# Kernel optimization log

Measured on AMD Instinct MI355X. Metric: run time of the kernel, lower is better.

## Reference

```python
import jax, jax.numpy as jnp
import numpy as np

DIM = 768
N_HEADS = 12
HEAD_DIM = DIM // N_HEADS

def setup_inputs() -> dict:
    key = jax.random.key(0)
    ks = jax.random.split(key, 5)
    B, N = 8, 1024
    s = 0.02
    x = jax.random.normal(ks[0], (B, N, DIM), dtype=jnp.float32)
    W_qkv = jax.random.normal(ks[1], (DIM, 3 * DIM), dtype=jnp.float32) * s
    b_qkv = jnp.zeros((3 * DIM,), dtype=jnp.float32)
    W_proj = jax.random.normal(ks[2], (DIM, DIM), dtype=jnp.float32) * s
    b_proj = jnp.zeros((DIM,), dtype=jnp.float32)
    return {"x": x, "W_qkv": W_qkv, "b_qkv": b_qkv, "W_proj": W_proj, "b_proj": b_proj}

def reference(x, W_qkv, b_qkv, W_proj, b_proj):
    B, N, D = x.shape
    qkv = x @ W_qkv + b_qkv                                   # [B,N,3D]
    qkv = qkv.reshape(B, N, 3, N_HEADS, HEAD_DIM)
    q, k, v = qkv[:, :, 0], qkv[:, :, 1], qkv[:, :, 2]        # [B,N,H,hd]
    q = q.transpose(0, 2, 1, 3)                               # [B,H,N,hd]
    k = k.transpose(0, 2, 1, 3)
    v = v.transpose(0, 2, 1, 3)
    scores = jnp.einsum('bhqd,bhkd->bhqk', q, k) / jnp.sqrt(jnp.float32(HEAD_DIM))
    attn = jax.nn.softmax(scores, axis=-1)
    out = jnp.einsum('bhqk,bhkd->bhqd', attn, v)              # [B,H,N,hd]
    out = out.transpose(0, 2, 1, 3).reshape(B, N, D)
    return out @ W_proj + b_proj
```

## Files before the change

### kernel.cpp

```cpp
#include <hip/hip_runtime.h>
#include <hip/hip_bf16.h>


typedef __bf16 bf16x8 __attribute__((ext_vector_type(8)));
typedef float f32x4 __attribute__((ext_vector_type(4)));

#define MFMA16(a, b, c) __builtin_amdgcn_mfma_f32_16x16x32_bf16(a, b, c, 0, 0, 0)

__device__ inline __bf16 to_bf16(float f) {
  __hip_bfloat16 h = __float2bfloat16(f);
  return *reinterpret_cast<__bf16*>(&h);
}

__device__ __forceinline__ void gload16(const void* g, void* l) {
  __builtin_amdgcn_global_load_lds(
      (const __attribute__((address_space(1))) unsigned int*)(unsigned long long)g,
      (__attribute__((address_space(3))) unsigned int*)(unsigned long long)l,
      16, 0, 0);
}

__global__ void ws_diag_kernel(float* out, int n, float val) {
  int i = blockIdx.x * 256 + threadIdx.x;
  if (i < n) out[i] = val;
}

__global__ __launch_bounds__(256) void convert_x_kernel(
    const float* __restrict__ x, __hip_bfloat16* __restrict__ xc, int n8) {
  int i = blockIdx.x * 256 + threadIdx.x;
  if (i >= n8) return;
  float4 a = ((const float4*)x)[i * 2], b = ((const float4*)x)[i * 2 + 1];
  __hip_bfloat16 o[8] = {__float2bfloat16(a.x), __float2bfloat16(a.y),
                         __float2bfloat16(a.z), __float2bfloat16(a.w),
                         __float2bfloat16(b.x), __float2bfloat16(b.y),
                         __float2bfloat16(b.z), __float2bfloat16(b.w)};
  *(int4*)(xc + (size_t)i * 8) = *(const int4*)o;
}

__global__ void convert_transpose_kernel(const float* __restrict__ W,
                                         __hip_bfloat16* __restrict__ Wt,
                                         int rows, int cols) {
  __shared__ __hip_bfloat16 tile[32][33];
  const int tc = blockIdx.x * 32, tr = blockIdx.y * 32;
  const int tx = threadIdx.x, ty = threadIdx.y;
#pragma unroll
  for (int i = 0; i < 4; ++i) {
    int r = ty + i * 8;
    tile[r][tx] = __float2bfloat16(W[(size_t)(tr + r) * cols + tc + tx]);
  }
  __syncthreads();
#pragma unroll
  for (int i = 0; i < 4; ++i) {
    int r = ty + i * 8;
    Wt[(size_t)(tc + r) * rows + tr + tx] = tile[tx][r];
  }
}

__global__ __launch_bounds__(256) void vtrans_kernel(
    const __hip_bfloat16* __restrict__ Vrow, __hip_bfloat16* __restrict__ Vt) {
  constexpr int LP = 72;
  __shared__ __bf16 tile[64 * LP];
  const int tid = threadIdx.x;
  const int bh = blockIdx.x;
  const int n0 = blockIdx.y * 64;
  const size_t base = (size_t)bh << 16;
#pragma unroll
  for (int i = 0; i < 2; ++i) {
    int s = tid + 256 * i;
    int r = s >> 3, c8 = (s & 7) * 8;
    *(int4*)(&tile[r * LP + c8]) =
        *(const int4*)(Vrow + base + (size_t)(n0 + r) * 64 + c8);
  }
  __syncthreads();
#pragma unroll
  for (int i = 0; i < 2; ++i) {
    int s = tid + 256 * i;
    int d = s >> 3, n8 = (s & 7) * 8;
    __bf16 o[8];
#pragma unroll
    for (int j = 0; j < 8; ++j) o[j] = tile[(n8 + j) * LP + d];
    *(int4*)(Vt + base + ((size_t)d << 10) + n0 + n8) = *(const int4*)o;
  }
}

constexpr int GK = 768;

__global__ __launch_bounds__(256) void gemm_qkv_kernel(
    const __hip_bfloat16* __restrict__ A,
    const __hip_bfloat16* __restrict__ Bt,
    const float* __restrict__ bias,
    __hip_bfloat16* __restrict__ Qw,
    __hip_bfloat16* __restrict__ Kw,
    __hip_bfloat16* __restrict__ Vw) {
  __shared__ __align__(16) __bf16 As[128 * 32];
  __shared__ __align__(16) __bf16 Bs[128 * 32];
  const int tid = threadIdx.x;
  const int lane = tid & 63, wave = tid >> 6;
  const int wr = wave >> 1, wc = wave & 1;
  const int m0 = blockIdx.x * 128, n0 = blockIdx.y * 128;
  const int fr = lane & 15, q4 = lane >> 4;

  const int r4 = lane >> 2, c8 = (lane & 3) * 8;
  const __hip_bfloat16* ga0 = A + (size_t)(m0 + wave * 32 + r4) * GK + c8;
  const __hip_bfloat16* gb0 = Bt + (size_t)(n0 + wave * 32 + r4) * GK + c8;
  __bf16* la0 = &As[wave * 1024];
  __bf16* lb0 = &Bs[wave * 1024];

  f32x4 acc[4][4] = {};

  for (int kt = 0; kt < GK / 32; ++kt) {
    __syncthreads();
    gload16(ga0 + kt * 32, la0);
    gload16(ga0 + kt * 32 + 16 * GK, la0 + 512);
    gload16(gb0 + kt * 32, lb0);
    gload16(gb0 + kt * 32 + 16 * GK, lb0 + 512);
    __syncthreads();
    bf16x8 af[4], bfr[4];
#pragma unroll
    for (int i = 0; i < 4; ++i)
      af[i] = *(const bf16x8*)(&As[(wr * 64 + i * 16 + fr) * 32 + q4 * 8]);
#pragma unroll
    for (int j = 0; j < 4; ++j)
      bfr[j] = *(const bf16x8*)(&Bs[(wc * 64 + j * 16 + fr) * 32 + q4 * 8]);
#pragma unroll
    for (int i = 0; i < 4; ++i)
#pragma unroll
      for (int j = 0; j < 4; ++j)
        acc[i][j] = MFMA16(af[i], bfr[j], acc[i][j]);
  }

#pragma unroll
  for (int j = 0; j < 4; ++j) {
    int col = n0 + wc * 64 + j * 16 + fr;
    int which = col / 768;
    int rem = col - which * 768;
    int h = rem >> 6, d = rem & 63;
    float bv = bias[col];
    __hip_bfloat16* dst = (which == 0) ? Qw : (which == 1) ? Kw : Vw;
    float scale = (which == 0) ? 0.18033688011112042f : 1.0f;
#pragma unroll
    for (int i = 0; i < 4; ++i) {
#pragma unroll
      for (int r = 0; r < 4; ++r) {
        int row = m0 + wr * 64 + i * 16 + q4 * 4 + r;
        int bb = row >> 10, nn = row & 1023;
        float v = (acc[i][j][r] + bv) * scale;
        dst[(((size_t)(bb * 12 + h) * 1024 + nn) << 6) + d] = __float2bfloat16(v);
      }
    }
  }
}

__global__ __launch_bounds__(256) void gemm_proj_kernel(
    const __hip_bfloat16* __restrict__ A,
    const __hip_bfloat16* __restrict__ Bt,
    const float* __restrict__ bias,
    float* __restrict__ out) {
  __shared__ __align__(16) __bf16 As[128 * 32];
  __shared__ __align__(16) __bf16 Bs[128 * 32];
  const int tid = threadIdx.x;
  const int lane = tid & 63, wave = tid >> 6;
  const int wr = wave >> 1, wc = wave & 1;
  const int m0 = blockIdx.x * 128, n0 = blockIdx.y * 128;
  const int fr = lane & 15, q4 = lane >> 4;

  const int r4 = lane >> 2, c8 = (lane & 3) * 8;
  const __hip_bfloat16* ga0 = A + (size_t)(m0 + wave * 32 + r4) * GK + c8;
  const __hip_bfloat16* gb0 = Bt + (size_t)(n0 + wave * 32 + r4) * GK + c8;
  __bf16* la0 = &As[wave * 1024];
  __bf16* lb0 = &Bs[wave * 1024];

  f32x4 acc[4][4] = {};

  for (int kt = 0; kt < GK / 32; ++kt) {
    __syncthreads();
    gload16(ga0 + kt * 32, la0);
    gload16(ga0 + kt * 32 + 16 * GK, la0 + 512);
    gload16(gb0 + kt * 32, lb0);
    gload16(gb0 + kt * 32 + 16 * GK, lb0 + 512);
    __syncthreads();
    bf16x8 af[4], bfr[4];
#pragma unroll
    for (int i = 0; i < 4; ++i)
      af[i] = *(const bf16x8*)(&As[(wr * 64 + i * 16 + fr) * 32 + q4 * 8]);
#pragma unroll
    for (int j = 0; j < 4; ++j)
      bfr[j] = *(const bf16x8*)(&Bs[(wc * 64 + j * 16 + fr) * 32 + q4 * 8]);
#pragma unroll
    for (int i = 0; i < 4; ++i)
#pragma unroll
      for (int j = 0; j < 4; ++j)
        acc[i][j] = MFMA16(af[i], bfr[j], acc[i][j]);
  }

#pragma unroll
  for (int j = 0; j < 4; ++j) {
    int col = n0 + wc * 64 + j * 16 + fr;
    float bv = bias[col];
#pragma unroll
    for (int i = 0; i < 4; ++i) {
#pragma unroll
      for (int r = 0; r < 4; ++r) {
        int row = m0 + wr * 64 + i * 16 + q4 * 4 + r;
        out[(size_t)row * 768 + col] = acc[i][j][r] + bv;
      }
    }
  }
}

__global__ __launch_bounds__(256) void attn_kernel(
    const __hip_bfloat16* __restrict__ Qw,
    const __hip_bfloat16* __restrict__ Kw,
    const __hip_bfloat16* __restrict__ Vt,
    __hip_bfloat16* __restrict__ O) {
  constexpr int LP = 72;
  __shared__ __bf16 Qs[128 * LP];
  __shared__ __bf16 Ks[64 * LP];
  __shared__ __bf16 Vts[64 * LP];
  const int tid = threadIdx.x;
  const int lane = tid & 63, wave = tid >> 6;
  const int fr = lane & 15, q4 = lane >> 4;
  const int bh = blockIdx.x % 96, qt = blockIdx.x / 96;
  const __hip_bfloat16* Qb = Qw + ((size_t)bh * 1024 + qt * 128) * 64;
  const __hip_bfloat16* Kb = Kw + (size_t)bh * 65536;
  const __hip_bfloat16* Vb = Vt + (size_t)bh * 65536;

  for (int s = tid; s < 1024; s += 256) {
    int row = s >> 3, c = (s & 7) * 8;
    *(int4*)(&Qs[row * LP + c]) = *(const int4*)(Qb + row * 64 + c);
  }
  __syncthreads();
  bf16x8 qf[2][2];
#pragma unroll
  for (int mt = 0; mt < 2; ++mt)
#pragma unroll
    for (int ks = 0; ks < 2; ++ks)
      qf[mt][ks] = *(const bf16x8*)(&Qs[(wave * 32 + mt * 16 + fr) * LP + ks * 32 + q4 * 8]);

  float l_i[2] = {};
  f32x4 accO[2][4] = {};

  const int sc8 = lane & 7;
  const int sbase = ((sc8 >> 2) << 5) | ((sc8 & 1) << 4) | (((sc8 >> 1) & 1) << 2);

  for (int kt = 0; kt < 16; ++kt) {
    int4 kreg[2], vreg[2];
#pragma unroll
    for (int i = 0; i < 2; ++i) {
      int s = tid + 256 * i;
      int row = s >> 3, c = (s & 7) * 8;
      kreg[i] = *(const int4*)(Kb + (size_t)(kt * 64 + row) * 64 + c);
      vreg[i] = *(const int4*)(Vb + ((size_t)row << 10) + kt * 64 + c);
    }
    __syncthreads();
#pragma unroll
    for (int i = 0; i < 2; ++i) {
      int s = tid + 256 * i;
      int row = s >> 3;
      *(int4*)(&Ks[row * LP + (s & 7) * 8]) = kreg[i];
      int2 lo = make_int2(vreg[i].x, vreg[i].y);
      int2 hi = make_int2(vreg[i].z, vreg[i].w);
      *(int2*)(&Vts[row * LP + sbase]) = lo;
      *(int2*)(&Vts[row * LP + sbase + 8]) = hi;
    }
    __syncthreads();

    f32x4 scT[2][4];
#pragma unroll
    for (int nt = 0; nt < 4; ++nt) {
      bf16x8 kf0 = *(const bf16x8*)(&Ks[(nt * 16 + fr) * LP + q4 * 8]);
      bf16x8 kf1 = *(const bf16x8*)(&Ks[(nt * 16 + fr) * LP + 32 + q4 * 8]);
#pragma unroll
      for (int mt = 0; mt < 2; ++mt) {
        f32x4 z = {};
        z = MFMA16(kf0, qf[mt][0], z);
        scT[mt][nt] = MFMA16(kf1, qf[mt][1], z);
      }
    }

#pragma unroll
    for (int mt = 0; mt < 2; ++mt) {
      float rs = 0.f;
#pragma unroll
      for (int nt = 0; nt < 4; ++nt)
#pragma unroll
        for (int r = 0; r < 4; ++r) {
          float p = exp2f(scT[mt][nt][r]);
          scT[mt][nt][r] = p;
          rs += p;
        }
      l_i[mt] += rs;
    }

#pragma unroll
    for (int ks = 0; ks < 2; ++ks) {
      bf16x8 pf[2];
#pragma unroll
      for (int mt = 0; mt < 2; ++mt) {
#pragma unroll
        for (int e = 0; e < 4; ++e) {
          pf[mt][e] = to_bf16(scT[mt][2 * ks][e]);
          pf[mt][4 + e] = to_bf16(scT[mt][2 * ks + 1][e]);
        }
      }
#pragma unroll
      for (int dt = 0; dt < 4; ++dt) {
        bf16x8 vf = *(const bf16x8*)(&Vts[(dt * 16 + fr) * LP + ks * 32 + q4 * 8]);
#pragma unroll
        for (int mt = 0; mt < 2; ++mt) accO[mt][dt] = MFMA16(pf[mt], vf, accO[mt][dt]);
      }
    }
  }

#pragma unroll
  for (int mt = 0; mt < 2; ++mt) {
    l_i[mt] += __shfl_xor(l_i[mt], 16, 64);
    l_i[mt] += __shfl_xor(l_i[mt], 32, 64);
  }
  float lrow[2][4];
#pragma unroll
  for (int mt = 0; mt < 2; ++mt)
#pragma unroll
    for (int r = 0; r < 4; ++r) lrow[mt][r] = __shfl(l_i[mt], q4 * 4 + r, 64);

  const int h = bh % 12, bb = bh / 12;
#pragma unroll
  for (int mt = 0; mt < 2; ++mt)
#pragma unroll
    for (int dt = 0; dt < 4; ++dt)
#pragma unroll
      for (int r = 0; r < 4; ++r) {
        int row = bb * 1024 + qt * 128 + wave * 32 + mt * 16 + q4 * 4 + r;
        int col = h * 64 + dt * 16 + fr;
        O[(size_t)row * 768 + col] = __float2bfloat16(accO[mt][dt][r] / lrow[mt][r]);
      }
}

extern "C" void kernel_launch(void* const* d_in, const int* in_sizes, int n_in,
                              void* d_out, int out_size, void* d_ws, size_t ws_size,
                              hipStream_t stream) {
  const float* x     = (const float*)d_in[0];
  const float* Wqkv  = (const float*)d_in[1];
  const float* bqkv  = (const float*)d_in[2];
  const float* Wproj = (const float*)d_in[3];
  const float* bproj = (const float*)d_in[4];
  float* out = (float*)d_out;

  constexpr size_t NEEDED = 55050240;
  if (ws_size < NEEDED) {
    ws_diag_kernel<<<(out_size + 255) / 256, 256, 0, stream>>>(
        out, out_size, (float)(ws_size >> 20));
    return;
  }

  char* ws = (char*)d_ws;
  __hip_bfloat16* WqkvT  = (__hip_bfloat16*)(ws);
  __hip_bfloat16* WprojT = (__hip_bfloat16*)(ws + 3538944);
  __hip_bfloat16* Qw     = (__hip_bfloat16*)(ws + 4718592);
  __hip_bfloat16* Kw     = (__hip_bfloat16*)(ws + 17301504);
  __hip_bfloat16* Vrow   = (__hip_bfloat16*)(ws + 29884416);
  __hip_bfloat16* xc     = (__hip_bfloat16*)(ws + 42467328);
  __hip_bfloat16* Vt     = xc;
  __hip_bfloat16* attnO  = Vrow;

  convert_x_kernel<<<3072, 256, 0, stream>>>(x, xc, 786432);
  convert_transpose_kernel<<<dim3(72, 24), dim3(32, 8), 0, stream>>>(
      Wqkv, WqkvT, 768, 2304);
  convert_transpose_kernel<<<dim3(24, 24), dim3(32, 8), 0, stream>>>(
      Wproj, WprojT, 768, 768);
  gemm_qkv_kernel<<<dim3(64, 18), 256, 0, stream>>>(xc, WqkvT, bqkv, Qw, Kw, Vrow);
  vtrans_kernel<<<dim3(96, 16), 256, 0, stream>>>(Vrow, Vt);
  attn_kernel<<<dim3(96 * 8), 256, 0, stream>>>(Qw, Kw, Vt, attnO);
  gemm_proj_kernel<<<dim3(64, 6), 256, 0, stream>>>(attnO, WprojT, bproj, out);
}
```

Before: 214.3 us.

## Split attention block work across eight waves and use native exp2 intrinsic

The attention kernel now launches 512 threads (8 waves) per block instead of 256, so each wave handles 16 query rows rather than 32. Each thread loads one K/V chunk per tile instead of two. Per-wave MFMA and exp work halves, which lowers register pressure and should help hide latency. The exp2f call becomes the raw AMDGPU exp2 builtin when available, skipping the libm wrapper. The trade-off is that each K/V tile loaded into shared memory is reused by fewer MFMAs per wave, while barrier overhead per block stays the same.

New measurement: 195.5 us. -8.8%, faster.

```diff
diff --git a/kernel.cpp b/kernel.cpp
--- a/kernel.cpp
+++ b/kernel.cpp
@@ -6,6 +6,12 @@
 typedef float f32x4 __attribute__((ext_vector_type(4)));
 
 #define MFMA16(a, b, c) __builtin_amdgcn_mfma_f32_16x16x32_bf16(a, b, c, 0, 0, 0)
+
+#if defined(__has_builtin) && __has_builtin(__builtin_amdgcn_exp2f)
+#define EXP2(x) __builtin_amdgcn_exp2f(x)
+#else
+#define EXP2(x) exp2f(x)
+#endif
 
 __device__ inline __bf16 to_bf16(float f) {
   __hip_bfloat16 h = __float2bfloat16(f);
@@ -207,7 +213,7 @@
   }
 }
 
-__global__ __launch_bounds__(256) void attn_kernel(
+__global__ __launch_bounds__(512) void attn_kernel(
     const __hip_bfloat16* __restrict__ Qw,
     const __hip_bfloat16* __restrict__ Kw,
     const __hip_bfloat16* __restrict__ Vt,
@@ -224,115 +230,88 @@
   const __hip_bfloat16* Kb = Kw + (size_t)bh * 65536;
   const __hip_bfloat16* Vb = Vt + (size_t)bh * 65536;
 
-  for (int s = tid; s < 1024; s += 256) {
+#pragma unroll
+  for (int i = 0; i < 2; ++i) {
+    int s = tid + 512 * i;
     int row = s >> 3, c = (s & 7) * 8;
     *(int4*)(&Qs[row * LP + c]) = *(const int4*)(Qb + row * 64 + c);
   }
   __syncthreads();
-  bf16x8 qf[2][2];
-#pragma unroll
-  for (int mt = 0; mt < 2; ++mt)
-#pragma unroll
-    for (int ks = 0; ks < 2; ++ks)
-      qf[mt][ks] = *(const bf16x8*)(&Qs[(wave * 32 + mt * 16 + fr) * LP + ks * 32 + q4 * 8]);
-
-  float l_i[2] = {};
-  f32x4 accO[2][4] = {};
-
-  const int sc8 = lane & 7;
+  bf16x8 qf[2];
+#pragma unroll
+  for (int ks = 0; ks < 2; ++ks)
+    qf[ks] = *(const bf16x8*)(&Qs[(wave * 16 + fr) * LP + ks * 32 + q4 * 8]);
+
+  float l_i = 0.f;
+  f32x4 accO[4] = {};
+
+  const int sc8 = tid & 7;
   const int sbase = ((sc8 >> 2) << 5) | ((sc8 & 1) << 4) | (((sc8 >> 1) & 1) << 2);
 
   for (int kt = 0; kt < 16; ++kt) {
-    int4 kreg[2], vreg[2];
-#pragma unroll
-    for (int i = 0; i < 2; ++i) {
-      int s = tid + 256 * i;
-      int row = s >> 3, c = (s & 7) * 8;
-      kreg[i] = *(const int4*)(Kb + (size_t)(kt * 64 + row) * 64 + c);
-      vreg[i] = *(const int4*)(Vb + ((size_t)row << 10) + kt * 64 + c);
-    }
-    __syncthreads();
-#pragma unroll
-    for (int i = 0; i < 2; ++i) {
-      int s = tid + 256 * i;
-      int row = s >> 3;
-      *(int4*)(&Ks[row * LP + (s & 7) * 8]) = kreg[i];
-      int2 lo = make_int2(vreg[i].x, vreg[i].y);
-      int2 hi = make_int2(vreg[i].z, vreg[i].w);
-      *(int2*)(&Vts[row * LP + sbase]) = lo;
-      *(int2*)(&Vts[row * LP + sbase + 8]) = hi;
-    }
-    __syncthreads();
-
-    f32x4 scT[2][4];
+    const int row = tid >> 3, c = (tid & 7) * 8;
+    int4 kreg = *(const int4*)(Kb + (size_t)(kt * 64 + row) * 64 + c);
+    int4 vreg = *(const int4*)(Vb + ((size_t)row << 10) + kt * 64 + c);
+    __syncthreads();
+    *(int4*)(&Ks[row * LP + c]) = kreg;
+    int2 lo = make_int2(vreg.x, vreg.y);
+    int2 hi = make_int2(vreg.z, vreg.w);
+    *(int2*)(&Vts[row * LP + sbase]) = lo;
+    *(int2*)(&Vts[row * LP + sbase + 8]) = hi;
+    __syncthreads();
+
+    f32x4 scT[4];
 #pragma unroll
     for (int nt = 0; nt < 4; ++nt) {
       bf16x8 kf0 = *(const bf16x8*)(&Ks[(nt * 16 + fr) * LP + q4 * 8]);
       bf16x8 kf1 = *(const bf16x8*)(&Ks[(nt * 16 + fr) * LP + 32 + q4 * 8]);
-#pragma unroll
-      for (int mt = 0; mt < 2; ++mt) {
-        f32x4 z = {};
-        z = MFMA16(kf0, qf[mt][0], z);
-        scT[mt][nt] = MFMA16(kf1, qf[mt][1], z);
-      }
-    }
-
-#pragma unroll
-    for (int mt = 0; mt < 2; ++mt) {
-      float rs = 0.f;
-#pragma unroll
-      for (int nt = 0; nt < 4; ++nt)
-#pragma unroll
-        for (int r = 0; r < 4; ++r) {
-          float p = exp2f(scT[mt][nt][r]);
-          scT[mt][nt][r] = p;
-          rs += p;
-        }
-      l_i[mt] += rs;
-    }
+      f32x4 z = {};
+      z = MFMA16(kf0, qf[0], z);
+      scT[nt] = MFMA16(kf1, qf[1], z);
+    }
+
+    float rs = 0.f;
+#pragma unroll
+    for (int nt = 0; nt < 4; ++nt)
+#pragma unroll
+      for (int r = 0; r < 4; ++r) {
+        float p = EXP2(scT[nt][r]);
+        scT[nt][r] = p;
+        rs += p;
+      }
+    l_i += rs;
 
 #pragma unroll
     for (int ks = 0; ks < 2; ++ks) {
-      bf16x8 pf[2];
-#pragma unroll
-      for (int mt = 0; mt < 2; ++mt) {
-#pragma unroll
-        for (int e = 0; e < 4; ++e) {
-          pf[mt][e] = to_bf16(scT[mt][2 * ks][e]);
-          pf[mt][4 + e] = to_bf16(scT[mt][2 * ks + 1][e]);
-        }
+      bf16x8 pf;
+#pragma unroll
+      for (int e = 0; e < 4; ++e) {
+        pf[e] = to_bf16(scT[2 * ks][e]);
+        pf[4 + e] = to_bf16(scT[2 * ks + 1][e]);
       }
 #pragma unroll
       for (int dt = 0; dt < 4; ++dt) {
         bf16x8 vf = *(const bf16x8*)(&Vts[(dt * 16 + fr) * LP + ks * 32 + q4 * 8]);
-#pragma unroll
-        for (int mt = 0; mt < 2; ++mt) accO[mt][dt] = MFMA16(pf[mt], vf, accO[mt][dt]);
-      }
-    }
-  }
-
-#pragma unroll
-  for (int mt = 0; mt < 2; ++mt) {
-    l_i[mt] += __shfl_xor(l_i[mt], 16, 64);
-    l_i[mt] += __shfl_xor(l_i[mt], 32, 64);
-  }
-  float lrow[2][4];
-#pragma unroll
-  for (int mt = 0; mt < 2; ++mt)
-#pragma unroll
-    for (int r = 0; r < 4; ++r) lrow[mt][r] = __shfl(l_i[mt], q4 * 4 + r, 64);
+        accO[dt] = MFMA16(pf, vf, accO[dt]);
+      }
+    }
+  }
+
+  l_i += __shfl_xor(l_i, 16, 64);
+  l_i += __shfl_xor(l_i, 32, 64);
+  float lrow[4];
+#pragma unroll
+  for (int r = 0; r < 4; ++r) lrow[r] = __shfl(l_i, q4 * 4 + r, 64);
 
   const int h = bh % 12, bb = bh / 12;
 #pragma unroll
-  for (int mt = 0; mt < 2; ++mt)
-#pragma unroll
-    for (int dt = 0; dt < 4; ++dt)
-#pragma unroll
-      for (int r = 0; r < 4; ++r) {
-        int row = bb * 1024 + qt * 128 + wave * 32 + mt * 16 + q4 * 4 + r;
-        int col = h * 64 + dt * 16 + fr;
-        O[(size_t)row * 768 + col] = __float2bfloat16(accO[mt][dt][r] / lrow[mt][r]);
-      }
+  for (int dt = 0; dt < 4; ++dt)
+#pragma unroll
+    for (int r = 0; r < 4; ++r) {
+      int row = bb * 1024 + qt * 128 + wave * 16 + q4 * 4 + r;
+      int col = h * 64 + dt * 16 + fr;
+      O[(size_t)row * 768 + col] = __float2bfloat16(accO[dt][r] / lrow[r]);
+    }
 }
 
 extern "C" void kernel_launch(void* const* d_in, const int* in_sizes, int n_in,
@@ -369,6 +348,6 @@
       Wproj, WprojT, 768, 768);
   gemm_qkv_kernel<<<dim3(64, 18), 256, 0, stream>>>(xc, WqkvT, bqkv, Qw, Kw, Vrow);
   vtrans_kernel<<<dim3(96, 16), 256, 0, stream>>>(Vrow, Vt);
-  attn_kernel<<<dim3(96 * 8), 256, 0, stream>>>(Qw, Kw, Vt, attnO);
+  attn_kernel<<<dim3(96 * 8), 512, 0, stream>>>(Qw, Kw, Vt, attnO);
   gemm_proj_kernel<<<dim3(64, 6), 256, 0, stream>>>(attnO, WprojT, bproj, out);
 }
```
